# Optimization experiments

Hardware: AMD Instinct MI355X
Metric: run time of the kernel (lower is better)

## Reference

```python
import jax, jax.numpy as jnp
import numpy as np

DIM = 384
EPS = 1e-12  # F.normalize default eps


def setup_inputs() -> dict:
    key = jax.random.key(0)
    ks = jax.random.split(key, 6)
    b, c, h, w = 4, DIM, 64, 64
    x = jax.random.normal(ks[0], (b, c, h, w), dtype=jnp.float32)
    gamma = jnp.ones((c,), dtype=jnp.float32)  # WanRMS_norm gamma, init ones
    # 1x1 convs are per-pixel linear maps: [out_c, in_c] weight + bias
    w_qkv = jax.random.normal(ks[1], (3 * c, c), dtype=jnp.float32) * (1.0 / np.sqrt(c))
    b_qkv = jax.random.normal(ks[2], (3 * c,), dtype=jnp.float32) * 0.01
    w_proj = jax.random.normal(ks[3], (c, c), dtype=jnp.float32) * (1.0 / np.sqrt(c))
    b_proj = jax.random.normal(ks[4], (c,), dtype=jnp.float32) * 0.01
    return {"x": x, "gamma": gamma, "w_qkv": w_qkv, "b_qkv": b_qkv,
            "w_proj": w_proj, "b_proj": b_proj}


def reference(x, gamma, w_qkv, b_qkv, w_proj, b_proj):
    b, c, h, w = x.shape
    identity = x
    # WanRMS_norm: F.normalize over channel dim * sqrt(dim) * gamma
    l2 = jnp.sqrt(jnp.sum(x * x, axis=1, keepdims=True))
    xn = x / jnp.maximum(l2, EPS) * jnp.sqrt(jnp.float32(c)) * gamma[None, :, None, None]
    # 1x1 conv qkv: [b, 3c, h, w]
    qkv = jnp.einsum("bchw,oc->bohw", xn, w_qkv) + b_qkv[None, :, None, None]
    # flatten spatial -> tokens: [b, 3c, s] -> q/k/v each [b, s, c]
    s = h * w
    qkv = qkv.reshape(b, 3 * c, s).transpose(0, 2, 1)  # [b, s, 3c]
    q, k, v = jnp.split(qkv, 3, axis=-1)
    # single-head scaled dot-product attention (non-causal, as in Wan SDPA call)
    scores = jnp.einsum("bqc,bkc->bqk", q, k) / jnp.sqrt(jnp.float32(c))
    attn = jax.nn.softmax(scores, axis=-1)
    out = jnp.einsum("bqk,bkc->bqc", attn, v)  # [b, s, c]
    out = out.transpose(0, 2, 1).reshape(b, c, h, w)
    # 1x1 proj conv + residual
    out = jnp.einsum("bchw,oc->bohw", out, w_proj) + b_proj[None, :, None, None]
    return out + identity
```

## Files before the change

### kernel.cpp

```cpp
#include <hip/hip_runtime.h>
#include <cstdint>
#include <cstddef>

typedef __bf16 bf16;
typedef __bf16 bf16x8 __attribute__((ext_vector_type(8)));
typedef float  f32x4 __attribute__((ext_vector_type(4)));
typedef float  f32x16 __attribute__((ext_vector_type(16)));
typedef int    i32x4 __attribute__((ext_vector_type(4)));
typedef int    i32x8 __attribute__((ext_vector_type(8)));

#define MFMA16(a, b, c) __builtin_amdgcn_mfma_f32_16x16x32_bf16((a), (b), (c), 0, 0, 0)
#define MFMA_MX(a, b, c) \
    __builtin_amdgcn_mfma_scale_f32_32x32x64_f8f6f4((a), (b), (c), 0, 0, 0, 0x7F, 0, 0x7F)

__device__ __forceinline__ uint8_t to_fp8(float v) {
    return (uint8_t)(__builtin_amdgcn_cvt_pk_fp8_f32(v, v, 0, false) & 0xff);
}

__device__ __forceinline__ i32x8 ld32(const void* p) {
    i32x4 a = *(const i32x4*)p;
    i32x4 b = *(const i32x4*)((const char*)p + 16);
    i32x8 r;
    r[0] = a[0]; r[1] = a[1]; r[2] = a[2]; r[3] = a[3];
    r[4] = b[0]; r[5] = b[1]; r[6] = b[2]; r[7] = b[3];
    return r;
}

__device__ __forceinline__ void gload16(const void* g, void* l) {
    __builtin_amdgcn_global_load_lds(
        (const __attribute__((address_space(1))) unsigned int*)g,
        (__attribute__((address_space(3))) unsigned int*)l,
        16, 0, 0);
}

__global__ __launch_bounds__(256) void norm_kernel(
    const float* __restrict__ x, const float* __restrict__ gamma,
    const float* __restrict__ wqkv, const float* __restrict__ wproj,
    bf16* __restrict__ xn, bf16* __restrict__ wq, bf16* __restrict__ wp)
{
    const int tid = threadIdx.x;
    const int blk = blockIdx.x;
    if (blk >= 256) {
        int t0 = (blk - 256) * 256 + tid;
        for (int t = t0; t < 1152 * 384 + 384 * 384; t += 128 * 256) {
            if (t < 1152 * 384) wq[t] = (bf16)wqkv[t];
            else                wp[t - 1152 * 384] = (bf16)wproj[t - 1152 * 384];
        }
        return;
    }
    __shared__ float sG[384];
    __shared__ float sS[4][64];
    __shared__ float sScale[64];
    const int w = tid >> 6, l = tid & 63;
    for (int i = tid; i < 384; i += 256) sG[i] = gamma[i];
    const int b = blk >> 6, p0 = (blk & 63) << 6;
    const float* xb = x + ((size_t)b * 384) * 4096 + p0 + l;
    const float* xc = xb + (size_t)(96 * w) * 4096;
    float s0 = 0.f, s1 = 0.f;
#pragma unroll 8
    for (int c = 0; c < 96; c += 2) {
        float v0 = xc[(size_t)c * 4096];
        float v1 = xc[(size_t)(c + 1) * 4096];
        s0 += v0 * v0; s1 += v1 * v1;
    }
    sS[w][l] = s0 + s1;
    __syncthreads();
    if (w == 0) {
        float t = (sS[0][l] + sS[1][l]) + (sS[2][l] + sS[3][l]);
        sScale[l] = 19.595917942265423f / fmaxf(sqrtf(t), 1e-12f);
    }
    __syncthreads();
    float sc = sScale[l];
    int tok = (b << 12) + p0 + l;
    bf16* o = xn + (size_t)tok * 384 + 96 * w;
    for (int c0 = 0; c0 < 96; c0 += 8) {
        bf16x8 v8;
#pragma unroll
        for (int j = 0; j < 8; ++j)
            v8[j] = (bf16)(xc[(size_t)(c0 + j) * 4096] * sc * sG[96 * w + c0 + j]);
        *(bf16x8*)(o + c0) = v8;
    }
}

__device__ __forceinline__ void gemm_core_bt(
    bf16* sA, bf16* sB,
    const bf16* __restrict__ A, const bf16* __restrict__ B,
    const float* __restrict__ bias_m, const float* __restrict__ bias_n,
    uint8_t* __restrict__ Cout, const int mode, const int ldc,
    const int m0, const int n0)
{
    const int tid = threadIdx.x;
    const int l = tid & 63, w = tid >> 6;
    const int lo = l & 15, hi = l >> 4;
    const int wm = w >> 1, wn = w & 1;

    f32x4 acc[4][4] = {};

    for (int kt = 0; kt < 6; ++kt) {
        __syncthreads();
        const int k0 = kt * 64;
#pragma unroll
        for (int i = 0; i < 5; ++i) {
            int ci = i * 256 + tid;
            if (ci < 1152) {
                int row = ci / 9, off = ci % 9;
                gload16(A + (size_t)(m0 + row) * 384 + k0 + off * 8, (char*)sA + ci * 16);
                gload16(B + (size_t)(n0 + row) * 384 + k0 + off * 8, (char*)sB + ci * 16);
            }
        }
        __syncthreads();
#pragma unroll
        for (int ks = 0; ks < 2; ++ks) {
            bf16x8 af[4], bfr[4];
#pragma unroll
            for (int t = 0; t < 4; ++t)
                af[t] = *(const bf16x8*)(sA + (wm * 64 + t * 16 + lo) * 72 + ks * 32 + hi * 8);
#pragma unroll
            for (int t = 0; t < 4; ++t)
                bfr[t] = *(const bf16x8*)(sB + (wn * 64 + t * 16 + lo) * 72 + ks * 32 + hi * 8);
#pragma unroll
            for (int rt = 0; rt < 4; ++rt)
#pragma unroll
                for (int ct = 0; ct < 4; ++ct)
                    acc[rt][ct] = MFMA16(af[rt], bfr[ct], acc[rt][ct]);
        }
    }

#pragma unroll
    for (int rt = 0; rt < 4; ++rt) {
#pragma unroll
        for (int ct = 0; ct < 4; ++ct) {
            int mb = m0 + wm * 64 + rt * 16 + hi * 4;
            int n  = n0 + wn * 64 + ct * 16 + lo;
            if (mode == 0) {
                float bn = bias_n[n];
#pragma unroll
                for (int r = 0; r < 4; ++r)
                    Cout[(size_t)(mb + r) * ldc + n] = to_fp8(acc[rt][ct][r] + bn);
            } else {
#pragma unroll
                for (int r = 0; r < 4; ++r)
                    Cout[(size_t)(mb + r) * ldc + n] = to_fp8(acc[rt][ct][r] + bias_m[mb + r]);
            }
        }
    }
}

__global__ __launch_bounds__(256) void gemm_qkv(
    const bf16* __restrict__ xn, const bf16* __restrict__ wq,
    const float* __restrict__ b_qkv, uint8_t* __restrict__ qkb,
    uint8_t* __restrict__ vtb)
{
    __shared__ bf16 sA[128 * 72];
    __shared__ bf16 sB[128 * 72];
    const int id = blockIdx.x;
    if (id < 768) {
        gemm_core_bt(sA, sB, xn, wq, nullptr, b_qkv, qkb, 0, 768,
                     (id / 6) * 128, (id % 6) * 128);
    } else {
        const int t = id - 768;
        gemm_core_bt(sA, sB, wq + (size_t)768 * 384, xn, b_qkv + 768, nullptr,
                     vtb, 1, 16384, (t >> 7) * 128, (t & 127) * 128);
    }
}

__global__ __launch_bounds__(256) void gemm_proj(
    const bf16* __restrict__ wp, const bf16* __restrict__ p0,
    const bf16* __restrict__ p1, const float* __restrict__ ml,
    const float* __restrict__ b_proj, const float* __restrict__ x,
    float* __restrict__ out)
{
    __shared__ bf16 sA[128 * 72];
    __shared__ bf16 sB[128 * 72];
    const int tid = threadIdx.x;
    const int l = tid & 63, w = tid >> 6;
    const int lo = l & 15, hi = l >> 4;
    const int wm = w >> 1, wn = w & 1;
    const int m0 = blockIdx.y * 128, n0 = blockIdx.x * 128;

    f32x4 acc[4][4] = {};

    for (int kt = 0; kt < 6; ++kt) {
        __syncthreads();
        const int k0 = kt * 64;
#pragma unroll
        for (int i = 0; i < 5; ++i) {
            int ci = i * 256 + tid;
            if (ci < 1152) {
                int row = ci / 9, off = ci % 9;
                gload16(wp + (size_t)(m0 + row) * 384 + k0 + off * 8, (char*)sA + ci * 16);
                int tok = n0 + row;
                float2 ml0 = *(const float2*)(ml + (size_t)tok * 2);
                float2 ml1 = *(const float2*)(ml + (size_t)(16384 + tok) * 2);
                float mM = fmaxf(ml0.x, ml1.x);
                float a0 = exp2f(ml0.x - mM), a1 = exp2f(ml1.x - mM);
                float inv = 1.0f / (a0 * ml0.y + a1 * ml1.y);
                float w0 = a0 * inv, w1 = a1 * inv;
                size_t boff = (size_t)tok * 384 + k0 + off * 8;
                bf16x8 v0 = *(const bf16x8*)(p0 + boff);
                bf16x8 v1 = *(const bf16x8*)(p1 + boff);
                bf16x8 r;
#pragma unroll
                for (int j = 0; j < 8; ++j)
                    r[j] = (bf16)((float)v0[j] * w0 + (float)v1[j] * w1);
                *(bf16x8*)((char*)sB + ci * 16) = r;
            }
        }
        __syncthreads();
#pragma unroll
        for (int ks = 0; ks < 2; ++ks) {
            bf16x8 af[4], bfr[4];
#pragma unroll
            for (int t = 0; t < 4; ++t)
                af[t] = *(const bf16x8*)(sA + (wm * 64 + t * 16 + lo) * 72 + ks * 32 + hi * 8);
#pragma unroll
            for (int t = 0; t < 4; ++t)
                bfr[t] = *(const bf16x8*)(sB + (wn * 64 + t * 16 + lo) * 72 + ks * 32 + hi * 8);
#pragma unroll
            for (int rt = 0; rt < 4; ++rt)
#pragma unroll
                for (int ct = 0; ct < 4; ++ct)
                    acc[rt][ct] = MFMA16(af[rt], bfr[ct], acc[rt][ct]);
        }
    }

#pragma unroll
    for (int rt = 0; rt < 4; ++rt) {
#pragma unroll
        for (int ct = 0; ct < 4; ++ct) {
            int mb = m0 + wm * 64 + rt * 16 + hi * 4;
            int n  = n0 + wn * 64 + ct * 16 + lo;
            int bb = n >> 12, p = n & 4095;
#pragma unroll
            for (int r = 0; r < 4; ++r) {
                int m = mb + r;
                size_t idx = ((size_t)(bb * 384 + m)) * 4096 + p;
                out[idx] = acc[rt][ct][r] + b_proj[m] + x[idx];
            }
        }
    }
}

__device__ __forceinline__ void stage_tiles64(
    const uint8_t* __restrict__ qk, const uint8_t* __restrict__ vt,
    int kv0, uint8_t* sK, uint8_t* sV, int tid)
{
    const uint8_t* kb = qk + (size_t)kv0 * 768 + 384;
#pragma unroll
    for (int i = 0; i < 7; ++i) {
        int ci = i * 256 + tid;
        if (ci < 1600) {
            int row = ci / 25, off = ci % 25;
            gload16(kb + (size_t)row * 768 + off * 16, sK + ci * 16);
        }
    }
    const uint8_t* vb = vt + kv0;
#pragma unroll
    for (int i = 0; i < 8; ++i) {
        int ci = i * 256 + tid;
        if (ci < 1920) {
            int row = ci / 5, off = ci % 5;
            gload16(vb + (size_t)row * 16384 + off * 16, sV + ci * 16);
        }
    }
}

__global__ __launch_bounds__(256, 2) void flash_kernel(
    const uint8_t* __restrict__ qk, const uint8_t* __restrict__ vt,
    bf16* __restrict__ op0, bf16* __restrict__ op1, float* __restrict__ ml)
{
    __shared__ char smem[56320];
    uint8_t* sK = (uint8_t*)smem;
    uint8_t* sV = (uint8_t*)smem + 25600;
    const int tid = threadIdx.x;
    const int l = tid & 63, w = tid >> 6;
    const int l31 = l & 31, hi2 = l >> 5;
    const int wq = w >> 1, wd = w & 1;
    const int id = blockIdx.x;
    const int qt = id >> 3, bh = id & 7;
    const int b = bh >> 1, half = bh & 1;
    const int q0 = b * 4096 + qt * 64;
    const int kvbase = b * 4096 + half * 2048;
    const float SC = 0.07362217057594547f;
    const float THR = 108.664f;

    i32x8 qf[6];
    {
        const uint8_t* qrow = qk + (size_t)(q0 + wq * 32 + l31) * 768 + hi2 * 32;
#pragma unroll
        for (int ksw = 0; ksw < 6; ++ksw)
            qf[ksw] = ld32(qrow + ksw * 64);
    }

    f32x16 o[6] = {};
    float m = -1e30f, lsum = 0.f;

    for (int kt = 0; kt < 32; ++kt) {
        stage_tiles64(qk, vt, kvbase + kt * 64, sK, sV, tid);
        __syncthreads();

        f32x16 s0 = {}, s1 = {};
        __builtin_amdgcn_s_setprio(1);
#pragma unroll
        for (int ksw = 0; ksw < 6; ++ksw) {
            i32x8 ak0 = ld32(sK + (size_t)l31 * 400 + ksw * 64 + hi2 * 32);
            i32x8 ak1 = ld32(sK + (size_t)(32 + l31) * 400 + ksw * 64 + hi2 * 32);
            s0 = MFMA_MX(ak0, qf[ksw], s0);
            s1 = MFMA_MX(ak1, qf[ksw], s1);
        }
        __builtin_amdgcn_s_setprio(0);

        float a0 = fmaxf(fmaxf(s0[0],  s0[1]),  fmaxf(s0[2],  s0[3]));
        float a1 = fmaxf(fmaxf(s0[4],  s0[5]),  fmaxf(s0[6],  s0[7]));
        float a2 = fmaxf(fmaxf(s0[8],  s0[9]),  fmaxf(s0[10], s0[11]));
        float a3 = fmaxf(fmaxf(s0[12], s0[13]), fmaxf(s0[14], s0[15]));
        float b0 = fmaxf(fmaxf(s1[0],  s1[1]),  fmaxf(s1[2],  s1[3]));
        float b1 = fmaxf(fmaxf(s1[4],  s1[5]),  fmaxf(s1[6],  s1[7]));
        float b2 = fmaxf(fmaxf(s1[8],  s1[9]),  fmaxf(s1[10], s1[11]));
        float b3 = fmaxf(fmaxf(s1[12], s1[13]), fmaxf(s1[14], s1[15]));
        float mx = fmaxf(fmaxf(fmaxf(a0, a1), fmaxf(a2, a3)),
                         fmaxf(fmaxf(b0, b1), fmaxf(b2, b3)));
        mx = fmaxf(mx, __shfl_xor(mx, 32));
        if (__any(mx > m + THR)) {
            float mn = fmaxf(m, mx);
            float alpha = exp2f((m - mn) * SC);
            m = mn;
            lsum *= alpha;
#pragma unroll
            for (int dt = 0; dt < 6; ++dt)
#pragma unroll
                for (int r = 0; r < 16; ++r) o[dt][r] *= alpha;
        }
        float p0[16], p1[16];
        float msc = m * SC;
        float rsa = 0.f, rsb = 0.f, rsc = 0.f, rsd = 0.f;
#pragma unroll
        for (int r = 0; r < 16; r += 4) {
            p0[r]     = exp2f(fmaf(s0[r],     SC, -msc)); rsa += p0[r];
            p0[r + 1] = exp2f(fmaf(s0[r + 1], SC, -msc)); rsb += p0[r + 1];
            p0[r + 2] = exp2f(fmaf(s0[r + 2], SC, -msc)); rsc += p0[r + 2];
            p0[r + 3] = exp2f(fmaf(s0[r + 3], SC, -msc)); rsd += p0[r + 3];
        }
#pragma unroll
        for (int r = 0; r < 16; r += 4) {
            p1[r]     = exp2f(fmaf(s1[r],     SC, -msc)); rsa += p1[r];
            p1[r + 1] = exp2f(fmaf(s1[r + 1], SC, -msc)); rsb += p1[r + 1];
            p1[r + 2] = exp2f(fmaf(s1[r + 2], SC, -msc)); rsc += p1[r + 2];
            p1[r + 3] = exp2f(fmaf(s1[r + 3], SC, -msc)); rsd += p1[r + 3];
        }
        float rs = (rsa + rsb) + (rsc + rsd);
        rs += __shfl_xor(rs, 32);
        lsum += rs;

        int pk0[4], pk1[4];
#pragma unroll
        for (int i = 0; i < 4; ++i) {
            int d = __builtin_amdgcn_cvt_pk_fp8_f32(p0[4 * i], p0[4 * i + 1], 0, false);
            pk0[i] = __builtin_amdgcn_cvt_pk_fp8_f32(p0[4 * i + 2], p0[4 * i + 3], d, true);
            d = __builtin_amdgcn_cvt_pk_fp8_f32(p1[4 * i], p1[4 * i + 1], 0, false);
            pk1[i] = __builtin_amdgcn_cvt_pk_fp8_f32(p1[4 * i + 2], p1[4 * i + 3], d, true);
        }
        i32x8 pf;
#pragma unroll
        for (int i = 0; i < 4; ++i) {
            int x0 = __shfl_xor(pk0[i], 32);
            int x1 = __shfl_xor(pk1[i], 32);
            int own = hi2 ? pk1[i] : pk0[i];
            int oth = hi2 ? x1 : x0;
            pf[2 * i]     = hi2 ? oth : own;
            pf[2 * i + 1] = hi2 ? own : oth;
        }

        __builtin_amdgcn_s_setprio(1);
#pragma unroll
        for (int dt = 0; dt < 6; ++dt) {
            i32x8 av = ld32(sV + (size_t)(wd * 192 + dt * 32 + l31) * 80 + hi2 * 32);
            o[dt] = MFMA_MX(av, pf, o[dt]);
        }
        __builtin_amdgcn_s_setprio(0);

        __syncthreads();
    }

    float* tr = (float*)(smem + w * 4608);
    bf16* dst = half ? op1 : op0;
#pragma unroll
    for (int dt = 0; dt < 6; ++dt) {
#pragma unroll
        for (int r = 0; r < 16; ++r) {
            int d32 = (r & 3) + 8 * (r >> 2) + 4 * hi2;
            tr[l31 * 36 + d32] = o[dt][r];
        }
        f32x4 v0 = *(f32x4*)(tr + l31 * 36 + hi2 * 16 + 0);
        f32x4 v1 = *(f32x4*)(tr + l31 * 36 + hi2 * 16 + 4);
        f32x4 v2 = *(f32x4*)(tr + l31 * 36 + hi2 * 16 + 8);
        f32x4 v3 = *(f32x4*)(tr + l31 * 36 + hi2 * 16 + 12);
        bf16x8 h0, h1;
#pragma unroll
        for (int j = 0; j < 4; ++j) {
            h0[j] = (bf16)v0[j]; h0[4 + j] = (bf16)v1[j];
            h1[j] = (bf16)v2[j]; h1[4 + j] = (bf16)v3[j];
        }
        size_t tok = (size_t)(q0 + wq * 32 + l31);
        bf16* drow = dst + tok * 384 + wd * 192 + dt * 32 + hi2 * 16;
        *(bf16x8*)(drow + 0) = h0;
        *(bf16x8*)(drow + 8) = h1;
        __syncthreads();
    }
    if (wd == 0 && hi2 == 0) {
        int tok = q0 + wq * 32 + l31;
        ml[(size_t)(half * 16384 + tok) * 2 + 0] = m * SC;
        ml[(size_t)(half * 16384 + tok) * 2 + 1] = lsum;
    }
}

extern "C" void kernel_launch(void* const* d_in, const int* in_sizes, int n_in,
                              void* d_out, int out_size, void* d_ws, size_t ws_size,
                              hipStream_t stream) {
    const float* x      = (const float*)d_in[0];
    const float* gamma  = (const float*)d_in[1];
    const float* w_qkv  = (const float*)d_in[2];
    const float* b_qkv  = (const float*)d_in[3];
    const float* w_proj = (const float*)d_in[4];
    const float* b_proj = (const float*)d_in[5];
    float* out = (float*)d_out;

    char* ws = (char*)d_ws;
    bf16* xn  = (bf16*)ws;    ws += (size_t)16384 * 384 * 2;
    uint8_t* qkb = (uint8_t*)ws; ws += (size_t)16384 * 768;
    uint8_t* vtb = (uint8_t*)ws; ws += (size_t)384 * 16384;
    bf16* ob  = (bf16*)ws;    ws += (size_t)16384 * 384 * 2;
    bf16* wqb = (bf16*)ws;    ws += (size_t)1152 * 384 * 2;
    bf16* wpb = (bf16*)ws;    ws += (size_t)384 * 384 * 2;
    float* mlb = (float*)ws;  ws += (size_t)2 * 16384 * 2 * 4;

    norm_kernel<<<384, 256, 0, stream>>>(x, gamma, w_qkv, w_proj, xn, wqb, wpb);
    gemm_qkv<<<1152, 256, 0, stream>>>(xn, wqb, b_qkv, qkb, vtb);
    flash_kernel<<<512, 256, 0, stream>>>(qkb, vtb, xn, ob, mlb);
    gemm_proj<<<dim3(128, 3), 256, 0, stream>>>(wpb, xn, ob, mlb, b_proj, x, out);
}
```

Baseline: 268.0 us.

## Double-buffer K tiles in flash kernel, XCD-aware GEMM block mapping, fast exp2

The flash attention kernel now double-buffers K tiles in dynamic shared memory, prefetching the next K tile while the current scores are computed. V for the current step loads alongside that work, with an extra barrier before the PV MFMAs. The QKV and projection GEMMs remap block IDs so that consecutive blocks on the same XCD share row or column tiles, aiming for better L2 reuse. exp2f calls switch to the hardware builtin. The risk is that 81920 bytes of shared memory per block may limit occupancy to fewer than the two blocks per CU the launch bounds request.

```diff
diff --git a/kernel.cpp b/kernel.cpp
--- a/kernel.cpp
+++ b/kernel.cpp
@@ -12,6 +12,12 @@
 #define MFMA16(a, b, c) __builtin_amdgcn_mfma_f32_16x16x32_bf16((a), (b), (c), 0, 0, 0)
 #define MFMA_MX(a, b, c) \
     __builtin_amdgcn_mfma_scale_f32_32x32x64_f8f6f4((a), (b), (c), 0, 0, 0, 0x7F, 0, 0x7F)
+
+#if __has_builtin(__builtin_amdgcn_exp2f)
+#define EXP2(x) __builtin_amdgcn_exp2f(x)
+#else
+#define EXP2(x) exp2f(x)
+#endif
 
 __device__ __forceinline__ uint8_t to_fp8(float v) {
     return (uint8_t)(__builtin_amdgcn_cvt_pk_fp8_f32(v, v, 0, false) & 0xff);
@@ -155,12 +161,14 @@
     __shared__ bf16 sB[128 * 72];
     const int id = blockIdx.x;
     if (id < 768) {
+        const int xcd = id & 7, s = id >> 3;
         gemm_core_bt(sA, sB, xn, wq, nullptr, b_qkv, qkb, 0, 768,
-                     (id / 6) * 128, (id % 6) * 128);
+                     (xcd * 16 + s / 6) * 128, (s % 6) * 128);
     } else {
         const int t = id - 768;
+        const int xcd = t & 7, s = t >> 3;
         gemm_core_bt(sA, sB, wq + (size_t)768 * 384, xn, b_qkv + 768, nullptr,
-                     vtb, 1, 16384, (t >> 7) * 128, (t & 127) * 128);
+                     vtb, 1, 16384, (s % 3) * 128, (xcd * 16 + s / 3) * 128);
     }
 }
 
@@ -176,7 +184,9 @@
     const int l = tid & 63, w = tid >> 6;
     const int lo = l & 15, hi = l >> 4;
     const int wm = w >> 1, wn = w & 1;
-    const int m0 = blockIdx.y * 128, n0 = blockIdx.x * 128;
+    const int id = blockIdx.x;
+    const int xcd = id & 7, s = id >> 3;
+    const int m0 = (s % 3) * 128, n0 = (xcd * 16 + s / 3) * 128;
 
     f32x4 acc[4][4] = {};
 
@@ -193,7 +203,7 @@
                 float2 ml0 = *(const float2*)(ml + (size_t)tok * 2);
                 float2 ml1 = *(const float2*)(ml + (size_t)(16384 + tok) * 2);
                 float mM = fmaxf(ml0.x, ml1.x);
-                float a0 = exp2f(ml0.x - mM), a1 = exp2f(ml1.x - mM);
+                float a0 = EXP2(ml0.x - mM), a1 = EXP2(ml1.x - mM);
                 float inv = 1.0f / (a0 * ml0.y + a1 * ml1.y);
                 float w0 = a0 * inv, w1 = a1 * inv;
                 size_t boff = (size_t)tok * 384 + k0 + off * 8;
@@ -241,9 +251,8 @@
     }
 }
 
-__device__ __forceinline__ void stage_tiles64(
-    const uint8_t* __restrict__ qk, const uint8_t* __restrict__ vt,
-    int kv0, uint8_t* sK, uint8_t* sV, int tid)
+__device__ __forceinline__ void stage_K64(
+    const uint8_t* __restrict__ qk, int kv0, uint8_t* dstK, int tid)
 {
     const uint8_t* kb = qk + (size_t)kv0 * 768 + 384;
 #pragma unroll
@@ -251,9 +260,14 @@
         int ci = i * 256 + tid;
         if (ci < 1600) {
             int row = ci / 25, off = ci % 25;
-            gload16(kb + (size_t)row * 768 + off * 16, sK + ci * 16);
-        }
-    }
+            gload16(kb + (size_t)row * 768 + off * 16, dstK + ci * 16);
+        }
+    }
+}
+
+__device__ __forceinline__ void stage_V64(
+    const uint8_t* __restrict__ vt, int kv0, uint8_t* sV, int tid)
+{
     const uint8_t* vb = vt + kv0;
 #pragma unroll
     for (int i = 0; i < 8; ++i) {
@@ -269,9 +283,9 @@
     const uint8_t* __restrict__ qk, const uint8_t* __restrict__ vt,
     bf16* __restrict__ op0, bf16* __restrict__ op1, float* __restrict__ ml)
 {
-    __shared__ char smem[56320];
-    uint8_t* sK = (uint8_t*)smem;
-    uint8_t* sV = (uint8_t*)smem + 25600;
+    extern __shared__ char smem[];
+    uint8_t* sbase = (uint8_t*)smem;
+    uint8_t* sV = sbase + 51200;
     const int tid = threadIdx.x;
     const int l = tid & 63, w = tid >> 6;
     const int l31 = l & 31, hi2 = l >> 5;
@@ -284,6 +298,8 @@
     const float SC = 0.07362217057594547f;
     const float THR = 108.664f;
 
+    stage_K64(qk, kvbase, sbase, tid);
+
     i32x8 qf[6];
     {
         const uint8_t* qrow = qk + (size_t)(q0 + wq * 32 + l31) * 768 + hi2 * 32;
@@ -295,10 +311,14 @@
     f32x16 o[6] = {};
     float m = -1e30f, lsum = 0.f;
 
+    __syncthreads();
+
+    int c = 0;
     for (int kt = 0; kt < 32; ++kt) {
-        stage_tiles64(qk, vt, kvbase + kt * 64, sK, sV, tid);
-        __syncthreads();
-
+        stage_V64(vt, kvbase + kt * 64, sV, tid);
+        if (kt < 31) stage_K64(qk, kvbase + (kt + 1) * 64, sbase + (c ^ 1) * 25600, tid);
+
+        uint8_t* sK = sbase + c * 25600;
         f32x16 s0 = {}, s1 = {};
         __builtin_amdgcn_s_setprio(1);
 #pragma unroll
@@ -323,7 +343,7 @@
         mx = fmaxf(mx, __shfl_xor(mx, 32));
         if (__any(mx > m + THR)) {
             float mn = fmaxf(m, mx);
-            float alpha = exp2f((m - mn) * SC);
+            float alpha = EXP2((m - mn) * SC);
             m = mn;
             lsum *= alpha;
 #pragma unroll
@@ -336,17 +356,17 @@
         float rsa = 0.f, rsb = 0.f, rsc = 0.f, rsd = 0.f;
 #pragma unroll
         for (int r = 0; r < 16; r += 4) {
-            p0[r]     = exp2f(fmaf(s0[r],     SC, -msc)); rsa += p0[r];
-            p0[r + 1] = exp2f(fmaf(s0[r + 1], SC, -msc)); rsb += p0[r + 1];
-            p0[r + 2] = exp2f(fmaf(s0[r + 2], SC, -msc)); rsc += p0[r + 2];
-            p0[r + 3] = exp2f(fmaf(s0[r + 3], SC, -msc)); rsd += p0[r + 3];
+            p0[r]     = EXP2(fmaf(s0[r],     SC, -msc)); rsa += p0[r];
+            p0[r + 1] = EXP2(fmaf(s0[r + 1], SC, -msc)); rsb += p0[r + 1];
+            p0[r + 2] = EXP2(fmaf(s0[r + 2], SC, -msc)); rsc += p0[r + 2];
+            p0[r + 3] = EXP2(fmaf(s0[r + 3], SC, -msc)); rsd += p0[r + 3];
         }
 #pragma unroll
         for (int r = 0; r < 16; r += 4) {
-            p1[r]     = exp2f(fmaf(s1[r],     SC, -msc)); rsa += p1[r];
-            p1[r + 1] = exp2f(fmaf(s1[r + 1], SC, -msc)); rsb += p1[r + 1];
-            p1[r + 2] = exp2f(fmaf(s1[r + 2], SC, -msc)); rsc += p1[r + 2];
-            p1[r + 3] = exp2f(fmaf(s1[r + 3], SC, -msc)); rsd += p1[r + 3];
+            p1[r]     = EXP2(fmaf(s1[r],     SC, -msc)); rsa += p1[r];
+            p1[r + 1] = EXP2(fmaf(s1[r + 1], SC, -msc)); rsb += p1[r + 1];
+            p1[r + 2] = EXP2(fmaf(s1[r + 2], SC, -msc)); rsc += p1[r + 2];
+            p1[r + 3] = EXP2(fmaf(s1[r + 3], SC, -msc)); rsd += p1[r + 3];
         }
         float rs = (rsa + rsb) + (rsc + rsd);
         rs += __shfl_xor(rs, 32);
@@ -371,6 +391,8 @@
             pf[2 * i + 1] = hi2 ? own : oth;
         }
 
+        __syncthreads();
+
         __builtin_amdgcn_s_setprio(1);
 #pragma unroll
         for (int dt = 0; dt < 6; ++dt) {
@@ -380,6 +402,7 @@
         __builtin_amdgcn_s_setprio(0);
 
         __syncthreads();
+        c ^= 1;
     }
 
     float* tr = (float*)(smem + w * 4608);
@@ -434,8 +457,11 @@
     bf16* wpb = (bf16*)ws;    ws += (size_t)384 * 384 * 2;
     float* mlb = (float*)ws;  ws += (size_t)2 * 16384 * 2 * 4;
 
+    (void)hipFuncSetAttribute((const void*)flash_kernel,
+                              hipFuncAttributeMaxDynamicSharedMemorySize, 81920);
+
     norm_kernel<<<384, 256, 0, stream>>>(x, gamma, w_qkv, w_proj, xn, wqb, wpb);
     gemm_qkv<<<1152, 256, 0, stream>>>(xn, wqb, b_qkv, qkb, vtb);
-    flash_kernel<<<512, 256, 0, stream>>>(qkb, vtb, xn, ob, mlb);
-    gemm_proj<<<dim3(128, 3), 256, 0, stream>>>(wpb, xn, ob, mlb, b_proj, x, out);
-}
+    flash_kernel<<<512, 256, 81920, stream>>>(qkb, vtb, xn, ob, mlb);
+    gemm_proj<<<384, 256, 0, stream>>>(wpb, xn, ob, mlb, b_proj, x, out);
+}
```

New measurement: 252.7 us. 1.06x faster.
